# Performance work log

Hardware: AMD Instinct MI355X
Metric: run time of the kernel (lower is better)

## Reference

```python
import jax, jax.numpy as jnp
import numpy as np

H_IMG, W_IMG = 32, 32   # image_size -> seq_len = 1024
NH, HD, D = 8, 32, 256  # num_heads, head_dim, d_model
B = 8


def _relative_positions(h, w):
    # Swin-style relative position index table, [h*w, h*w] int32
    y = np.arange(h); x = np.arange(w)
    coords = np.stack(np.meshgrid(y, x, indexing='ij')).reshape(2, -1)  # [2, S]
    rel = coords[:, :, None] - coords[:, None, :]                      # [2, S, S]
    rel = rel.transpose(1, 2, 0).astype(np.int64)                      # [S, S, 2]
    rel[:, :, 0] += h - 1
    rel[:, :, 1] += w - 1
    rel[:, :, 0] *= 2 * w - 1
    return np.int32(rel.sum(-1))                                       # [S, S]

_POS = _relative_positions(H_IMG, W_IMG)


def setup_inputs() -> dict:
    key = jax.random.key(0)
    ks = jax.random.split(key, 8)
    S = H_IMG * W_IMG
    return {
        'inputs_q': jax.random.normal(ks[0], (B, S, D), jnp.float32),
        'inputs_kv': jax.random.normal(ks[1], (B, S, D), jnp.float32),
        'Wq': jax.random.normal(ks[2], (D, NH, HD), jnp.float32) / np.sqrt(D),
        'bq': jnp.zeros((NH, HD), jnp.float32),
        'Wk': jax.random.normal(ks[3], (D, NH, HD), jnp.float32) / np.sqrt(D),
        'bk': jnp.zeros((NH, HD), jnp.float32),
        'Wv': jax.random.normal(ks[4], (D, NH, HD), jnp.float32) / np.sqrt(D),
        'bv': jnp.zeros((NH, HD), jnp.float32),
        'rel_table': 0.02 * jax.random.normal(ks[5], ((2 * H_IMG - 1) * (2 * W_IMG - 1), NH), jnp.float32),
        'Wo': jax.random.normal(ks[6], (NH, HD, D), jnp.float32) / np.sqrt(NH * HD),
        'bo': jnp.zeros((D,), jnp.float32),
    }


def reference(inputs_q, inputs_kv, Wq, bq, Wk, bk, Wv, bv, rel_table, Wo, bo):
    pos = jnp.asarray(_POS)                                  # [S, S] int32 (constant)
    q = jnp.einsum('bsd,dhk->bshk', inputs_q, Wq) + bq       # [B, S, H, HD]
    k = jnp.einsum('bsd,dhk->bshk', inputs_kv, Wk) + bk
    v = jnp.einsum('bsd,dhk->bshk', inputs_kv, Wv) + bv
    q = q / jnp.sqrt(jnp.asarray(HD, q.dtype))
    attn = jnp.einsum('bqhd,bkhd->bhqk', q, k)               # [B, H, S, S]
    rel_bias = rel_table[pos]                                # [S, S, H]
    attn = attn + jnp.transpose(rel_bias, (2, 0, 1))[None]   # broadcast over batch
    attn = jax.nn.softmax(attn, axis=-1)
    x = jnp.einsum('bhqk,bkhd->bqhd', attn, v)               # [B, S, H, HD]
    return jnp.einsum('bqhd,hdf->bqf', x, Wo) + bo           # [B, S, D]
```

## Files before the change

kernel.cpp:

```cpp
#include <hip/hip_runtime.h>

#define B_SZ   8
#define S_LEN  1024
#define D_MOD  256
#define NHEADS 8
#define M_ROWS 8192
#define LOG2E  1.4426950408889634f
#define QSCALE_LOG2E 0.2550352766751165f

typedef _Float16 f16x8 __attribute__((ext_vector_type(8)));
typedef _Float16 f16x4 __attribute__((ext_vector_type(4)));
typedef float    f32x4 __attribute__((ext_vector_type(4)));

__global__ __launch_bounds__(256)
void prep_kernel(const float* __restrict__ Wq, const float* __restrict__ Wk,
                 const float* __restrict__ Wv, const float* __restrict__ Wo,
                 const float* __restrict__ rel,
                 _Float16* __restrict__ wtp, float* __restrict__ tab) {
    if (blockIdx.x < 32) {
        __shared__ _Float16 Wl[32 * 264];
        const int mi = blockIdx.x >> 3;
        const int k0 = (blockIdx.x & 7) << 5;
        const float* W = (mi == 0) ? Wq : (mi == 1) ? Wk : (mi == 2) ? Wv : Wo;
        {
            const int r  = threadIdx.x >> 3;
            const int c4 = (threadIdx.x & 7) * 4;
            const float* src = W + (size_t)(k0 + r) * 256 + c4;
#pragma unroll
            for (int g = 0; g < 8; ++g) {
                f32x4 v = *(const f32x4*)(src + g * 32);
                f16x4 o;
#pragma unroll
                for (int j = 0; j < 4; ++j) o[j] = (_Float16)v[j];
                *(f16x4*)(&Wl[r * 264 + c4 + g * 32]) = o;
            }
        }
        __syncthreads();
        const int n16 = threadIdx.x >> 4;
        const int l16 = threadIdx.x & 15;
        const int kk  = k0 >> 5;
#pragma unroll
        for (int quad = 0; quad < 4; ++quad) {
            f16x8 v;
#pragma unroll
            for (int j = 0; j < 8; ++j) v[j] = Wl[(quad * 8 + j) * 264 + n16 * 16 + l16];
            *(f16x8*)(wtp + (((size_t)(mi * 16 + n16) * 8 + kk) << 9) + (quad * 16 + l16) * 8) = v;
        }
        return;
    }
    __shared__ float rl[63 * 8];
    const int dy31 = blockIdx.x - 32;
    for (int f = threadIdx.x; f < 504; f += 256) rl[f] = rel[(size_t)dy31 * 504 + f];
    __syncthreads();
    const int h  = threadIdx.x >> 5;
    const int r5 = threadIdx.x & 31;
#pragma unroll
    for (int c = 0; c < 6; ++c) {
        const int oi   = r5 * 6 + c;
        const int e    = oi >> 6;
        const int lane = oi & 63;
        const int quad = lane >> 4, l16 = lane & 15;
        f32x4 v;
#pragma unroll
        for (int reg = 0; reg < 4; ++reg) {
            const int idx = 16 * e + l16 - quad * 4 - reg + 15;
            v[reg] = rl[idx * 8 + h] * LOG2E;
        }
        *(f32x4*)(tab + (((size_t)(h * 63 + dy31) * 3 + e) << 8) + lane * 4) = v;
    }
}

__global__ __launch_bounds__(256)
void gemm_qkv_kernel(const float* __restrict__ in_q, const float* __restrict__ in_kv,
                     const _Float16* __restrict__ wtp,
                     const float* __restrict__ bq, const float* __restrict__ bk,
                     const float* __restrict__ bv,
                     _Float16* __restrict__ qs, _Float16* __restrict__ ks,
                     _Float16* __restrict__ vs) {
    __shared__ __align__(16) _Float16 As[64 * 264];
    _Float16* Ta = As;
    _Float16* Tb = As + 64 * 72;

    const int tid  = threadIdx.x;
    const int w    = tid >> 6;
    const int lane = tid & 63;
    const int quad = lane >> 4;
    const int l16  = lane & 15;
    const int m0 = blockIdx.x * 64, n0 = blockIdx.y * 64, z = blockIdx.z;
    const int b = m0 >> 10, mloc = m0 & 1023;

    {
        const int r  = tid >> 2;
        const int c4 = (tid & 3) * 4;
        const float* src = (z ? in_kv : in_q) + (size_t)(m0 + r) * 256 + c4;
        _Float16* dst = As + r * 264 + c4;
#pragma unroll
        for (int g = 0; g < 16; ++g) {
            f32x4 v = *(const f32x4*)(src + g * 16);
            f16x4 o;
#pragma unroll
            for (int j = 0; j < 4; ++j) o[j] = (_Float16)v[j];
            *(f16x4*)(dst + g * 16) = o;
        }
    }
    __syncthreads();

    const int n16base = (n0 >> 4) + (w >> 1) * 2;
    const int mA = z ? 1 : 0;
    const _Float16* wA0 = wtp + (((size_t)(mA * 16 + n16base + 0) * 8) << 9) + lane * 8;
    const _Float16* wA1 = wtp + (((size_t)(mA * 16 + n16base + 1) * 8) << 9) + lane * 8;
    const _Float16* wV0 = wtp + (((size_t)(2 * 16 + n16base + 0) * 8) << 9) + lane * 8;
    const _Float16* wV1 = wtp + (((size_t)(2 * 16 + n16base + 1) * 8) << 9) + lane * 8;
    const _Float16* arow0 = As + ((w & 1) * 32 + l16) * 264;
    const _Float16* arow1 = arow0 + 16 * 264;

    f32x4 accA[2][2], accV[2][2];
#pragma unroll
    for (int i = 0; i < 2; ++i)
#pragma unroll
        for (int j = 0; j < 2; ++j) {
            accA[i][j] = (f32x4){0.f, 0.f, 0.f, 0.f};
            accV[i][j] = (f32x4){0.f, 0.f, 0.f, 0.f};
        }

#pragma unroll
    for (int kk = 0; kk < 8; ++kk) {
        const int k8 = kk * 32 + quad * 8;
        f16x8 a0 = *(const f16x8*)(arow0 + k8);
        f16x8 a1 = *(const f16x8*)(arow1 + k8);
        f16x8 w0 = *(const f16x8*)(wA0 + kk * 512);
        f16x8 w1 = *(const f16x8*)(wA1 + kk * 512);
        accA[0][0] = __builtin_amdgcn_mfma_f32_16x16x32_f16(w0, a0, accA[0][0], 0, 0, 0);
        accA[0][1] = __builtin_amdgcn_mfma_f32_16x16x32_f16(w0, a1, accA[0][1], 0, 0, 0);
        accA[1][0] = __builtin_amdgcn_mfma_f32_16x16x32_f16(w1, a0, accA[1][0], 0, 0, 0);
        accA[1][1] = __builtin_amdgcn_mfma_f32_16x16x32_f16(w1, a1, accA[1][1], 0, 0, 0);
        if (z == 1) {
            f16x8 v0 = *(const f16x8*)(wV0 + kk * 512);
            f16x8 v1 = *(const f16x8*)(wV1 + kk * 512);
            accV[0][0] = __builtin_amdgcn_mfma_f32_16x16x32_f16(a0, v0, accV[0][0], 0, 0, 0);
            accV[0][1] = __builtin_amdgcn_mfma_f32_16x16x32_f16(a0, v1, accV[0][1], 0, 0, 0);
            accV[1][0] = __builtin_amdgcn_mfma_f32_16x16x32_f16(a1, v0, accV[1][0], 0, 0, 0);
            accV[1][1] = __builtin_amdgcn_mfma_f32_16x16x32_f16(a1, v1, accV[1][1], 0, 0, 0);
        }
    }
    __syncthreads();

    {
        const float* biasA = z ? bk : bq;
        const float  sc    = z ? 1.0f : QSCALE_LOG2E;
#pragma unroll
        for (int i = 0; i < 2; ++i) {
            f32x4 b4 = *(const f32x4*)(biasA + n0 + (w >> 1) * 32 + i * 16 + quad * 4);
#pragma unroll
            for (int jj = 0; jj < 2; ++jj) {
                f16x4 pk;
#pragma unroll
                for (int r = 0; r < 4; ++r) pk[r] = (_Float16)((accA[i][jj][r] + b4[r]) * sc);
                *(f16x4*)(Ta + ((w & 1) * 32 + jj * 16 + l16) * 72 +
                               (w >> 1) * 32 + i * 16 + quad * 4) = pk;
            }
        }
        if (z == 1) {
#pragma unroll
            for (int i = 0; i < 2; ++i) {
                const float bvv = bv[n0 + (w >> 1) * 32 + i * 16 + l16];
#pragma unroll
                for (int jj = 0; jj < 2; ++jj) {
                    f16x4 pk;
#pragma unroll
                    for (int r = 0; r < 4; ++r) pk[r] = (_Float16)(accV[jj][i][r] + bvv);
                    *(f16x4*)(Tb + ((w >> 1) * 32 + i * 16 + l16) * 72 +
                                   (w & 1) * 32 + jj * 16 + quad * 4) = pk;
                }
            }
        }
    }
    __syncthreads();
    {
        const int l16c = tid & 15, qdc = (tid >> 4) & 3;
        const int tile0 = mloc >> 5;
#pragma unroll
        for (int c2i = 0; c2i < 2; ++c2i) {
            const int c2 = w * 2 + c2i;
            const int s2 = c2 >> 2, sub = (c2 >> 1) & 1, hs = c2 & 1;
            const int bh = b * 8 + (n0 >> 5) + hs;
            const size_t dbase = (((size_t)(bh * 32 + tile0 + s2) * 2 + sub) << 9) + lane * 8;
            f16x8 va = *(const f16x8*)(Ta + (s2 * 32 + sub * 16 + l16c) * 72 +
                                            hs * 32 + qdc * 8);
            *(f16x8*)((z ? ks : qs) + dbase) = va;
            if (z == 1) {
                f16x8 vb = *(const f16x8*)(Tb + (hs * 32 + sub * 16 + l16c) * 72 +
                                                s2 * 32 + qdc * 8);
                *(f16x8*)(vs + dbase) = vb;
            }
        }
    }
}

__global__ __launch_bounds__(256)
void gemm_out_kernel(const _Float16* __restrict__ xh, const _Float16* __restrict__ wtp,
                     const float* __restrict__ bo, float* __restrict__ out) {
    __shared__ __align__(16) _Float16 As[64 * 264];
    const int tid  = threadIdx.x;
    const int w    = tid >> 6;
    const int lane = tid & 63;
    const int quad = lane >> 4;
    const int l16  = lane & 15;
    const int m0 = blockIdx.x * 64, n0 = blockIdx.y * 64;

    {
        const int r  = tid >> 2;
        const int c8 = (tid & 3) * 8;
        const _Float16* src = xh + (size_t)(m0 + r) * 256 + c8;
        _Float16* dst = As + r * 264 + c8;
#pragma unroll
        for (int g = 0; g < 8; ++g)
            *(f16x8*)(dst + g * 32) = *(const f16x8*)(src + g * 32);
    }
    __syncthreads();

    const int n16base = 48 + (n0 >> 4) + (w >> 1) * 2;
    const _Float16* w0p = wtp + (((size_t)(n16base + 0) * 8) << 9) + lane * 8;
    const _Float16* w1p = wtp + (((size_t)(n16base + 1) * 8) << 9) + lane * 8;
    const _Float16* arow0 = As + ((w & 1) * 32 + l16) * 264;
    const _Float16* arow1 = arow0 + 16 * 264;

    f32x4 acc[2][2];
#pragma unroll
    for (int i = 0; i < 2; ++i)
#pragma unroll
        for (int j = 0; j < 2; ++j) acc[i][j] = (f32x4){0.f, 0.f, 0.f, 0.f};

#pragma unroll
    for (int kk = 0; kk < 8; ++kk) {
        const int k8 = kk * 32 + quad * 8;
        f16x8 a0 = *(const f16x8*)(arow0 + k8);
        f16x8 a1 = *(const f16x8*)(arow1 + k8);
        f16x8 b0 = *(const f16x8*)(w0p + kk * 512);
        f16x8 b1 = *(const f16x8*)(w1p + kk * 512);
        acc[0][0] = __builtin_amdgcn_mfma_f32_16x16x32_f16(a0, b0, acc[0][0], 0, 0, 0);
        acc[0][1] = __builtin_amdgcn_mfma_f32_16x16x32_f16(a0, b1, acc[0][1], 0, 0, 0);
        acc[1][0] = __builtin_amdgcn_mfma_f32_16x16x32_f16(a1, b0, acc[1][0], 0, 0, 0);
        acc[1][1] = __builtin_amdgcn_mfma_f32_16x16x32_f16(a1, b1, acc[1][1], 0, 0, 0);
    }

#pragma unroll
    for (int i = 0; i < 2; ++i) {
        const int col = n0 + (w >> 1) * 32 + i * 16 + l16;
        const float bvv = bo[col];
#pragma unroll
        for (int jj = 0; jj < 2; ++jj) {
#pragma unroll
            for (int r = 0; r < 4; ++r) {
                const int row = m0 + (w & 1) * 32 + jj * 16 + quad * 4 + r;
                out[(size_t)row * 256 + col] = acc[jj][i][r] + bvv;
            }
        }
    }
}

__global__ __launch_bounds__(256)
void attn_kernel(const _Float16* __restrict__ qs, const _Float16* __restrict__ ks,
                 const _Float16* __restrict__ vs, const float* __restrict__ tab,
                 _Float16* __restrict__ xh) {
    __shared__ __align__(16) _Float16 Ps[4][32][40];

    const int tid  = threadIdx.x;
    const int w    = tid >> 6;
    const int lane = tid & 63;
    const int quad = lane >> 4;
    const int l16  = lane & 15;

    const int n     = blockIdx.x;
    const int xcd   = n & 7;
    const int local = n >> 3;
    const int bh    = xcd * 8 + (local & 7);
    const int qc    = local >> 3;
    const int b = bh >> 3, h = bh & 7;
    const int qrow_base = qc * 128 + w * 32;
    const int yq = qc * 4 + w;

    const _Float16* qp = qs + (((size_t)(bh * 32 + yq) * 2) << 9) + lane * 8;
    const f16x8 qf0 = *(const f16x8*)(qp);
    const f16x8 qf1 = *(const f16x8*)(qp + 512);
    const _Float16* kp = ks + (((size_t)bh * 64) << 9) + lane * 8;
    const _Float16* vp = vs + (((size_t)bh * 64) << 9) + lane * 8;
    const float* tb = tab + (((size_t)h * 63 * 3) << 8) + lane * 4;

    f16x8 ones;
#pragma unroll
    for (int j = 0; j < 8; ++j) ones[j] = (_Float16)1.0f;

    f32x4 o00 = {0.f,0.f,0.f,0.f}, o01 = {0.f,0.f,0.f,0.f};
    f32x4 o10 = {0.f,0.f,0.f,0.f}, o11 = {0.f,0.f,0.f,0.f};
    f32x4 ol0 = {0.f,0.f,0.f,0.f}, ol1 = {0.f,0.f,0.f,0.f};

    f16x8 kf0 = *(const f16x8*)(kp);
    f16x8 kf1 = *(const f16x8*)(kp + 512);
    f16x8 vf0 = *(const f16x8*)(vp);
    f16x8 vf1 = *(const f16x8*)(vp + 512);
    f32x4 c0 = *(const f32x4*)(tb + (yq + 31) * 768);
    f32x4 c1 = *(const f32x4*)(tb + (yq + 31) * 768 + 256);
    f32x4 c2 = *(const f32x4*)(tb + (yq + 31) * 768 + 512);

    for (int kt = 0; kt < 32; ++kt) {
        const bool more = (kt < 31);
        f16x8 nk0, nk1, nv0, nv1;
        f32x4 nc0, nc1, nc2;
        if (more) {
            const _Float16* kq = kp + (kt + 1) * 1024;
            nk0 = *(const f16x8*)(kq);
            nk1 = *(const f16x8*)(kq + 512);
            const _Float16* vq = vp + (kt + 1) * 1024;
            nv0 = *(const f16x8*)(vq);
            nv1 = *(const f16x8*)(vq + 512);
            const int d = (yq + 30 - kt) * 768;
            nc0 = *(const f32x4*)(tb + d);
            nc1 = *(const f32x4*)(tb + d + 256);
            nc2 = *(const f32x4*)(tb + d + 512);
        }

        f32x4 s00 = __builtin_amdgcn_mfma_f32_16x16x32_f16(kf0, qf0, c1, 0, 0, 0);
        f32x4 s01 = __builtin_amdgcn_mfma_f32_16x16x32_f16(kf1, qf0, c0, 0, 0, 0);
        f32x4 s10 = __builtin_amdgcn_mfma_f32_16x16x32_f16(kf0, qf1, c2, 0, 0, 0);
        f32x4 s11 = __builtin_amdgcn_mfma_f32_16x16x32_f16(kf1, qf1, c1, 0, 0, 0);

        f16x4 p;
#pragma unroll
        for (int r = 0; r < 4; ++r) p[r] = (_Float16)__builtin_amdgcn_exp2f(s00[r]);
        *(f16x4*)(&Ps[w][l16][quad * 4]) = p;
#pragma unroll
        for (int r = 0; r < 4; ++r) p[r] = (_Float16)__builtin_amdgcn_exp2f(s01[r]);
        *(f16x4*)(&Ps[w][l16][16 + quad * 4]) = p;
#pragma unroll
        for (int r = 0; r < 4; ++r) p[r] = (_Float16)__builtin_amdgcn_exp2f(s10[r]);
        *(f16x4*)(&Ps[w][16 + l16][quad * 4]) = p;
#pragma unroll
        for (int r = 0; r < 4; ++r) p[r] = (_Float16)__builtin_amdgcn_exp2f(s11[r]);
        *(f16x4*)(&Ps[w][16 + l16][16 + quad * 4]) = p;

        const f16x8 pf0 = *(const f16x8*)(&Ps[w][l16][quad * 8]);
        const f16x8 pf1 = *(const f16x8*)(&Ps[w][16 + l16][quad * 8]);
        o00 = __builtin_amdgcn_mfma_f32_16x16x32_f16(vf0, pf0, o00, 0, 0, 0);
        o01 = __builtin_amdgcn_mfma_f32_16x16x32_f16(vf0, pf1, o01, 0, 0, 0);
        o10 = __builtin_amdgcn_mfma_f32_16x16x32_f16(vf1, pf0, o10, 0, 0, 0);
        o11 = __builtin_amdgcn_mfma_f32_16x16x32_f16(vf1, pf1, o11, 0, 0, 0);
        ol0 = __builtin_amdgcn_mfma_f32_16x16x32_f16(ones, pf0, ol0, 0, 0, 0);
        ol1 = __builtin_amdgcn_mfma_f32_16x16x32_f16(ones, pf1, ol1, 0, 0, 0);

        if (more) {
            kf0 = nk0; kf1 = nk1; vf0 = nv0; vf1 = nv1;
            c0 = nc0; c1 = nc1; c2 = nc2;
        }
    }

#pragma unroll
    for (int qh = 0; qh < 2; ++qh) {
        const f32x4 onl = qh ? o01 : o00;
        const f32x4 onh = qh ? o11 : o10;
        const f32x4 ll  = qh ? ol1 : ol0;
        const float inv = __builtin_amdgcn_rcpf(ll[0]);
        const int qg = qrow_base + qh * 16 + l16;
        f16x4 u, v;
#pragma unroll
        for (int r = 0; r < 4; ++r) {
            u[r] = (_Float16)(onl[r] * inv);
            v[r] = (_Float16)(onh[r] * inv);
        }
        _Float16* op = xh + ((size_t)(b * S_LEN + qg)) * D_MOD + h * 32 + quad * 4;
        *(f16x4*)(op)      = u;
        *(f16x4*)(op + 16) = v;
    }
}

extern "C" void kernel_launch(void* const* d_in, const int* in_sizes, int n_in,
                              void* d_out, int out_size, void* d_ws, size_t ws_size,
                              hipStream_t stream) {
    const float* in_q  = (const float*)d_in[0];
    const float* in_kv = (const float*)d_in[1];
    const float* Wq    = (const float*)d_in[2];
    const float* bq    = (const float*)d_in[3];
    const float* Wk    = (const float*)d_in[4];
    const float* bk    = (const float*)d_in[5];
    const float* Wv    = (const float*)d_in[6];
    const float* bv    = (const float*)d_in[7];
    const float* rel   = (const float*)d_in[8];
    const float* Wo    = (const float*)d_in[9];
    const float* bo    = (const float*)d_in[10];
    float* out = (float*)d_out;

    char* wsb = (char*)d_ws;
    _Float16* qs  = (_Float16*)(wsb);
    _Float16* ks  = (_Float16*)(wsb + (size_t)4  * 1048576);
    _Float16* vs  = (_Float16*)(wsb + (size_t)8  * 1048576);
    _Float16* xh  = (_Float16*)(wsb + (size_t)12 * 1048576);
    _Float16* wtp = (_Float16*)(wsb + (size_t)16 * 1048576);
    float*    tab = (float*)   (wsb + (size_t)17 * 1048576);

    const dim3 blk(256);

    prep_kernel<<<dim3(95), blk, 0, stream>>>(Wq, Wk, Wv, Wo, rel, wtp, tab);
    gemm_qkv_kernel<<<dim3(128, 4, 2), blk, 0, stream>>>(
        in_q, in_kv, wtp, bq, bk, bv, qs, ks, vs);
    attn_kernel<<<dim3(512), blk, 0, stream>>>(qs, ks, vs, tab, xh);
    gemm_out_kernel<<<dim3(128, 4), blk, 0, stream>>>(xh, wtp, bo, out);
}
```

Baseline: 124.1 us.

## Store bias table in fp16, retile QKV GEMM, write attention output in MFMA layout

The relative-position bias table is now stored in fp16 and converted to float inside the attention loop, which halves the bytes it reads per tile. The QKV projection is retiled so each block handles 32 rows across the full 256 output columns for one of Q, K or V, on a grid of 256 by 3. The attention kernel now writes its output already packed in MFMA fragment order, so the output GEMM can read fragments straight from global memory and no longer stages them in LDS. The costs are some extra conversion instructions in the attention loop and fp16 rounding of the bias values.

Measured after the change: 127.3 us. 2.6% more time.

```diff
diff --git a/kernel.cpp b/kernel.cpp
--- a/kernel.cpp
+++ b/kernel.cpp
@@ -4,7 +4,6 @@
 #define S_LEN  1024
 #define D_MOD  256
 #define NHEADS 8
-#define M_ROWS 8192
 #define LOG2E  1.4426950408889634f
 #define QSCALE_LOG2E 0.2550352766751165f
 
@@ -16,7 +15,7 @@
 void prep_kernel(const float* __restrict__ Wq, const float* __restrict__ Wk,
                  const float* __restrict__ Wv, const float* __restrict__ Wo,
                  const float* __restrict__ rel,
-                 _Float16* __restrict__ wtp, float* __restrict__ tab) {
+                 _Float16* __restrict__ wtp, _Float16* __restrict__ tabh) {
     if (blockIdx.x < 32) {
         __shared__ _Float16 Wl[32 * 264];
         const int mi = blockIdx.x >> 3;
@@ -60,13 +59,13 @@
         const int e    = oi >> 6;
         const int lane = oi & 63;
         const int quad = lane >> 4, l16 = lane & 15;
-        f32x4 v;
+        f16x4 v;
 #pragma unroll
         for (int reg = 0; reg < 4; ++reg) {
             const int idx = 16 * e + l16 - quad * 4 - reg + 15;
-            v[reg] = rl[idx * 8 + h] * LOG2E;
-        }
-        *(f32x4*)(tab + (((size_t)(h * 63 + dy31) * 3 + e) << 8) + lane * 4) = v;
+            v[reg] = (_Float16)(rl[idx * 8 + h] * LOG2E);
+        }
+        *(f16x4*)(tabh + (((size_t)(h * 63 + dy31) * 3 + e) << 8) + lane * 4) = v;
     }
 }
 
@@ -77,153 +76,115 @@
                      const float* __restrict__ bv,
                      _Float16* __restrict__ qs, _Float16* __restrict__ ks,
                      _Float16* __restrict__ vs) {
-    __shared__ __align__(16) _Float16 As[64 * 264];
-    _Float16* Ta = As;
-    _Float16* Tb = As + 64 * 72;
-
+    __shared__ __align__(16) _Float16 Lds[256 * 40];
     const int tid  = threadIdx.x;
     const int w    = tid >> 6;
     const int lane = tid & 63;
     const int quad = lane >> 4;
     const int l16  = lane & 15;
-    const int m0 = blockIdx.x * 64, n0 = blockIdx.y * 64, z = blockIdx.z;
-    const int b = m0 >> 10, mloc = m0 & 1023;
+    const int mt = blockIdx.x;
+    const int z  = blockIdx.y;
+    const int m0 = mt * 32;
+    const int b  = mt >> 5, t = mt & 31;
 
     {
-        const int r  = tid >> 2;
-        const int c4 = (tid & 3) * 4;
+        const int r  = tid >> 3;
+        const int c4 = (tid & 7) * 4;
         const float* src = (z ? in_kv : in_q) + (size_t)(m0 + r) * 256 + c4;
-        _Float16* dst = As + r * 264 + c4;
-#pragma unroll
-        for (int g = 0; g < 16; ++g) {
-            f32x4 v = *(const f32x4*)(src + g * 16);
+        _Float16* dst = Lds + r * 264 + c4;
+#pragma unroll
+        for (int g = 0; g < 8; ++g) {
+            f32x4 v = *(const f32x4*)(src + g * 32);
             f16x4 o;
 #pragma unroll
             for (int j = 0; j < 4; ++j) o[j] = (_Float16)v[j];
-            *(f16x4*)(dst + g * 16) = o;
+            *(f16x4*)(dst + g * 32) = o;
         }
     }
     __syncthreads();
 
-    const int n16base = (n0 >> 4) + (w >> 1) * 2;
-    const int mA = z ? 1 : 0;
-    const _Float16* wA0 = wtp + (((size_t)(mA * 16 + n16base + 0) * 8) << 9) + lane * 8;
-    const _Float16* wA1 = wtp + (((size_t)(mA * 16 + n16base + 1) * 8) << 9) + lane * 8;
-    const _Float16* wV0 = wtp + (((size_t)(2 * 16 + n16base + 0) * 8) << 9) + lane * 8;
-    const _Float16* wV1 = wtp + (((size_t)(2 * 16 + n16base + 1) * 8) << 9) + lane * 8;
-    const _Float16* arow0 = As + ((w & 1) * 32 + l16) * 264;
-    const _Float16* arow1 = arow0 + 16 * 264;
-
-    f32x4 accA[2][2], accV[2][2];
-#pragma unroll
-    for (int i = 0; i < 2; ++i)
-#pragma unroll
-        for (int j = 0; j < 2; ++j) {
-            accA[i][j] = (f32x4){0.f, 0.f, 0.f, 0.f};
-            accV[i][j] = (f32x4){0.f, 0.f, 0.f, 0.f};
-        }
+    f32x4 acc[2][4];
+#pragma unroll
+    for (int jj = 0; jj < 2; ++jj)
+#pragma unroll
+        for (int i = 0; i < 4; ++i) acc[jj][i] = (f32x4){0.f, 0.f, 0.f, 0.f};
 
 #pragma unroll
     for (int kk = 0; kk < 8; ++kk) {
         const int k8 = kk * 32 + quad * 8;
-        f16x8 a0 = *(const f16x8*)(arow0 + k8);
-        f16x8 a1 = *(const f16x8*)(arow1 + k8);
-        f16x8 w0 = *(const f16x8*)(wA0 + kk * 512);
-        f16x8 w1 = *(const f16x8*)(wA1 + kk * 512);
-        accA[0][0] = __builtin_amdgcn_mfma_f32_16x16x32_f16(w0, a0, accA[0][0], 0, 0, 0);
-        accA[0][1] = __builtin_amdgcn_mfma_f32_16x16x32_f16(w0, a1, accA[0][1], 0, 0, 0);
-        accA[1][0] = __builtin_amdgcn_mfma_f32_16x16x32_f16(w1, a0, accA[1][0], 0, 0, 0);
-        accA[1][1] = __builtin_amdgcn_mfma_f32_16x16x32_f16(w1, a1, accA[1][1], 0, 0, 0);
-        if (z == 1) {
-            f16x8 v0 = *(const f16x8*)(wV0 + kk * 512);
-            f16x8 v1 = *(const f16x8*)(wV1 + kk * 512);
-            accV[0][0] = __builtin_amdgcn_mfma_f32_16x16x32_f16(a0, v0, accV[0][0], 0, 0, 0);
-            accV[0][1] = __builtin_amdgcn_mfma_f32_16x16x32_f16(a0, v1, accV[0][1], 0, 0, 0);
-            accV[1][0] = __builtin_amdgcn_mfma_f32_16x16x32_f16(a1, v0, accV[1][0], 0, 0, 0);
-            accV[1][1] = __builtin_amdgcn_mfma_f32_16x16x32_f16(a1, v1, accV[1][1], 0, 0, 0);
+        f16x8 a0 = *(const f16x8*)(Lds + l16 * 264 + k8);
+        f16x8 a1 = *(const f16x8*)(Lds + (16 + l16) * 264 + k8);
+#pragma unroll
+        for (int i = 0; i < 4; ++i) {
+            f16x8 wv = *(const f16x8*)(wtp + (((size_t)(z * 16 + w * 4 + i) * 8 + kk) << 9) + lane * 8);
+            if (z < 2) {
+                acc[0][i] = __builtin_amdgcn_mfma_f32_16x16x32_f16(wv, a0, acc[0][i], 0, 0, 0);
+                acc[1][i] = __builtin_amdgcn_mfma_f32_16x16x32_f16(wv, a1, acc[1][i], 0, 0, 0);
+            } else {
+                acc[0][i] = __builtin_amdgcn_mfma_f32_16x16x32_f16(a0, wv, acc[0][i], 0, 0, 0);
+                acc[1][i] = __builtin_amdgcn_mfma_f32_16x16x32_f16(a1, wv, acc[1][i], 0, 0, 0);
+            }
         }
     }
     __syncthreads();
 
-    {
-        const float* biasA = z ? bk : bq;
-        const float  sc    = z ? 1.0f : QSCALE_LOG2E;
-#pragma unroll
-        for (int i = 0; i < 2; ++i) {
-            f32x4 b4 = *(const f32x4*)(biasA + n0 + (w >> 1) * 32 + i * 16 + quad * 4);
+    if (z < 2) {
+        const float* bias = z ? bk : bq;
+        const float  sc   = z ? 1.0f : QSCALE_LOG2E;
+#pragma unroll
+        for (int i = 0; i < 4; ++i) {
+            f32x4 b4 = *(const f32x4*)(bias + (w * 4 + i) * 16 + quad * 4);
 #pragma unroll
             for (int jj = 0; jj < 2; ++jj) {
                 f16x4 pk;
 #pragma unroll
-                for (int r = 0; r < 4; ++r) pk[r] = (_Float16)((accA[i][jj][r] + b4[r]) * sc);
-                *(f16x4*)(Ta + ((w & 1) * 32 + jj * 16 + l16) * 72 +
-                               (w >> 1) * 32 + i * 16 + quad * 4) = pk;
-            }
-        }
-        if (z == 1) {
-#pragma unroll
-            for (int i = 0; i < 2; ++i) {
-                const float bvv = bv[n0 + (w >> 1) * 32 + i * 16 + l16];
-#pragma unroll
-                for (int jj = 0; jj < 2; ++jj) {
-                    f16x4 pk;
-#pragma unroll
-                    for (int r = 0; r < 4; ++r) pk[r] = (_Float16)(accV[jj][i][r] + bvv);
-                    *(f16x4*)(Tb + ((w >> 1) * 32 + i * 16 + l16) * 72 +
-                                   (w & 1) * 32 + jj * 16 + quad * 4) = pk;
-                }
-            }
-        }
-    }
-    __syncthreads();
-    {
-        const int l16c = tid & 15, qdc = (tid >> 4) & 3;
-        const int tile0 = mloc >> 5;
-#pragma unroll
-        for (int c2i = 0; c2i < 2; ++c2i) {
-            const int c2 = w * 2 + c2i;
-            const int s2 = c2 >> 2, sub = (c2 >> 1) & 1, hs = c2 & 1;
-            const int bh = b * 8 + (n0 >> 5) + hs;
-            const size_t dbase = (((size_t)(bh * 32 + tile0 + s2) * 2 + sub) << 9) + lane * 8;
-            f16x8 va = *(const f16x8*)(Ta + (s2 * 32 + sub * 16 + l16c) * 72 +
-                                            hs * 32 + qdc * 8);
-            *(f16x8*)((z ? ks : qs) + dbase) = va;
-            if (z == 1) {
-                f16x8 vb = *(const f16x8*)(Tb + (hs * 32 + sub * 16 + l16c) * 72 +
-                                                s2 * 32 + qdc * 8);
-                *(f16x8*)(vs + dbase) = vb;
-            }
+                for (int r = 0; r < 4; ++r) pk[r] = (_Float16)((acc[jj][i][r] + b4[r]) * sc);
+                *(f16x4*)(Lds + (jj * 16 + l16) * 264 + (w * 4 + i) * 16 + quad * 4) = pk;
+            }
+        }
+        __syncthreads();
+        _Float16* dst = z ? ks : qs;
+#pragma unroll
+        for (int c = 0; c < 4; ++c) {
+            const int sg = w * 4 + c;
+            const int sub = sg >> 3, h = sg & 7;
+            f16x8 v = *(const f16x8*)(Lds + (sub * 16 + l16) * 264 + h * 32 + quad * 8);
+            *(f16x8*)(dst + (((size_t)((b * 8 + h) * 32 + t) * 2 + sub) << 9) + lane * 8) = v;
+        }
+    } else {
+#pragma unroll
+        for (int i = 0; i < 4; ++i) {
+            const float bvv = bv[(w * 4 + i) * 16 + l16];
+#pragma unroll
+            for (int jj = 0; jj < 2; ++jj) {
+                f16x4 pk;
+#pragma unroll
+                for (int r = 0; r < 4; ++r) pk[r] = (_Float16)(acc[jj][i][r] + bvv);
+                *(f16x4*)(Lds + ((w * 4 + i) * 16 + l16) * 40 + jj * 16 + quad * 4) = pk;
+            }
+        }
+        __syncthreads();
+#pragma unroll
+        for (int c = 0; c < 4; ++c) {
+            const int sg = w * 4 + c;
+            const int sub = sg >> 3, h = sg & 7;
+            f16x8 v = *(const f16x8*)(Lds + (h * 32 + sub * 16 + l16) * 40 + quad * 8);
+            *(f16x8*)(vs + (((size_t)((b * 8 + h) * 32 + t) * 2 + sub) << 9) + lane * 8) = v;
         }
     }
 }
 
 __global__ __launch_bounds__(256)
-void gemm_out_kernel(const _Float16* __restrict__ xh, const _Float16* __restrict__ wtp,
+void gemm_out_kernel(const _Float16* __restrict__ xs, const _Float16* __restrict__ wtp,
                      const float* __restrict__ bo, float* __restrict__ out) {
-    __shared__ __align__(16) _Float16 As[64 * 264];
     const int tid  = threadIdx.x;
     const int w    = tid >> 6;
     const int lane = tid & 63;
     const int quad = lane >> 4;
     const int l16  = lane & 15;
-    const int m0 = blockIdx.x * 64, n0 = blockIdx.y * 64;
-
-    {
-        const int r  = tid >> 2;
-        const int c8 = (tid & 3) * 8;
-        const _Float16* src = xh + (size_t)(m0 + r) * 256 + c8;
-        _Float16* dst = As + r * 264 + c8;
-#pragma unroll
-        for (int g = 0; g < 8; ++g)
-            *(f16x8*)(dst + g * 32) = *(const f16x8*)(src + g * 32);
-    }
-    __syncthreads();
-
-    const int n16base = 48 + (n0 >> 4) + (w >> 1) * 2;
-    const _Float16* w0p = wtp + (((size_t)(n16base + 0) * 8) << 9) + lane * 8;
-    const _Float16* w1p = wtp + (((size_t)(n16base + 1) * 8) << 9) + lane * 8;
-    const _Float16* arow0 = As + ((w & 1) * 32 + l16) * 264;
-    const _Float16* arow1 = arow0 + 16 * 264;
+    const int bx = blockIdx.x, by = blockIdx.y;
+    const int mt0  = bx * 4 + (w & 1) * 2;
+    const int n16a = by * 4 + (w >> 1) * 2;
 
     f32x4 acc[2][2];
 #pragma unroll
@@ -233,11 +194,10 @@
 
 #pragma unroll
     for (int kk = 0; kk < 8; ++kk) {
-        const int k8 = kk * 32 + quad * 8;
-        f16x8 a0 = *(const f16x8*)(arow0 + k8);
-        f16x8 a1 = *(const f16x8*)(arow1 + k8);
-        f16x8 b0 = *(const f16x8*)(w0p + kk * 512);
-        f16x8 b1 = *(const f16x8*)(w1p + kk * 512);
+        f16x8 a0 = *(const f16x8*)(xs + (((size_t)(mt0 + 0) * 8 + kk) << 9) + lane * 8);
+        f16x8 a1 = *(const f16x8*)(xs + (((size_t)(mt0 + 1) * 8 + kk) << 9) + lane * 8);
+        f16x8 b0 = *(const f16x8*)(wtp + (((size_t)(48 + n16a + 0) * 8 + kk) << 9) + lane * 8);
+        f16x8 b1 = *(const f16x8*)(wtp + (((size_t)(48 + n16a + 1) * 8 + kk) << 9) + lane * 8);
         acc[0][0] = __builtin_amdgcn_mfma_f32_16x16x32_f16(a0, b0, acc[0][0], 0, 0, 0);
         acc[0][1] = __builtin_amdgcn_mfma_f32_16x16x32_f16(a0, b1, acc[0][1], 0, 0, 0);
         acc[1][0] = __builtin_amdgcn_mfma_f32_16x16x32_f16(a1, b0, acc[1][0], 0, 0, 0);
@@ -246,13 +206,13 @@
 
 #pragma unroll
     for (int i = 0; i < 2; ++i) {
-        const int col = n0 + (w >> 1) * 32 + i * 16 + l16;
+        const int col = (n16a + i) * 16 + l16;
         const float bvv = bo[col];
 #pragma unroll
         for (int jj = 0; jj < 2; ++jj) {
 #pragma unroll
             for (int r = 0; r < 4; ++r) {
-                const int row = m0 + (w & 1) * 32 + jj * 16 + quad * 4 + r;
+                const int row = (mt0 + jj) * 16 + quad * 4 + r;
                 out[(size_t)row * 256 + col] = acc[jj][i][r] + bvv;
             }
         }
@@ -261,8 +221,8 @@
 
 __global__ __launch_bounds__(256)
 void attn_kernel(const _Float16* __restrict__ qs, const _Float16* __restrict__ ks,
-                 const _Float16* __restrict__ vs, const float* __restrict__ tab,
-                 _Float16* __restrict__ xh) {
+                 const _Float16* __restrict__ vs, const _Float16* __restrict__ tabh,
+                 _Float16* __restrict__ xs) {
     __shared__ __align__(16) _Float16 Ps[4][32][40];
 
     const int tid  = threadIdx.x;
@@ -285,7 +245,7 @@
     const f16x8 qf1 = *(const f16x8*)(qp + 512);
     const _Float16* kp = ks + (((size_t)bh * 64) << 9) + lane * 8;
     const _Float16* vp = vs + (((size_t)bh * 64) << 9) + lane * 8;
-    const float* tb = tab + (((size_t)h * 63 * 3) << 8) + lane * 4;
+    const _Float16* tb = tabh + (((size_t)h * 189) << 8) + lane * 4;
 
     f16x8 ones;
 #pragma unroll
@@ -299,14 +259,21 @@
     f16x8 kf1 = *(const f16x8*)(kp + 512);
     f16x8 vf0 = *(const f16x8*)(vp);
     f16x8 vf1 = *(const f16x8*)(vp + 512);
-    f32x4 c0 = *(const f32x4*)(tb + (yq + 31) * 768);
-    f32x4 c1 = *(const f32x4*)(tb + (yq + 31) * 768 + 256);
-    f32x4 c2 = *(const f32x4*)(tb + (yq + 31) * 768 + 512);
+    f32x4 c0, c1, c2;
+    {
+        f16x4 t0 = *(const f16x4*)(tb + (((yq + 31) * 3 + 0) << 8));
+        f16x4 t1 = *(const f16x4*)(tb + (((yq + 31) * 3 + 1) << 8));
+        f16x4 t2 = *(const f16x4*)(tb + (((yq + 31) * 3 + 2) << 8));
+#pragma unroll
+        for (int r = 0; r < 4; ++r) {
+            c0[r] = (float)t0[r]; c1[r] = (float)t1[r]; c2[r] = (float)t2[r];
+        }
+    }
 
     for (int kt = 0; kt < 32; ++kt) {
         const bool more = (kt < 31);
         f16x8 nk0, nk1, nv0, nv1;
-        f32x4 nc0, nc1, nc2;
+        f16x4 nt0, nt1, nt2;
         if (more) {
             const _Float16* kq = kp + (kt + 1) * 1024;
             nk0 = *(const f16x8*)(kq);
@@ -314,10 +281,10 @@
             const _Float16* vq = vp + (kt + 1) * 1024;
             nv0 = *(const f16x8*)(vq);
             nv1 = *(const f16x8*)(vq + 512);
-            const int d = (yq + 30 - kt) * 768;
-            nc0 = *(const f32x4*)(tb + d);
-            nc1 = *(const f32x4*)(tb + d + 256);
-            nc2 = *(const f32x4*)(tb + d + 512);
+            const int d = (yq + 30 - kt) * 3;
+            nt0 = *(const f16x4*)(tb + ((d + 0) << 8));
+            nt1 = *(const f16x4*)(tb + ((d + 1) << 8));
+            nt2 = *(const f16x4*)(tb + ((d + 2) << 8));
         }
 
         f32x4 s00 = __builtin_amdgcn_mfma_f32_16x16x32_f16(kf0, qf0, c1, 0, 0, 0);
@@ -350,26 +317,33 @@
 
         if (more) {
             kf0 = nk0; kf1 = nk1; vf0 = nv0; vf1 = nv1;
-            c0 = nc0; c1 = nc1; c2 = nc2;
-        }
-    }
-
-#pragma unroll
-    for (int qh = 0; qh < 2; ++qh) {
-        const f32x4 onl = qh ? o01 : o00;
-        const f32x4 onh = qh ? o11 : o10;
-        const f32x4 ll  = qh ? ol1 : ol0;
+#pragma unroll
+            for (int r = 0; r < 4; ++r) {
+                c0[r] = (float)nt0[r]; c1[r] = (float)nt1[r]; c2[r] = (float)nt2[r];
+            }
+        }
+    }
+
+#pragma unroll
+    for (int qsub = 0; qsub < 2; ++qsub) {
+        const f32x4 olo = qsub ? o01 : o00;
+        const f32x4 ohi = qsub ? o11 : o10;
+        const f32x4 ll  = qsub ? ol1 : ol0;
         const float inv = __builtin_amdgcn_rcpf(ll[0]);
-        const int qg = qrow_base + qh * 16 + l16;
         f16x4 u, v;
 #pragma unroll
         for (int r = 0; r < 4; ++r) {
-            u[r] = (_Float16)(onl[r] * inv);
-            v[r] = (_Float16)(onh[r] * inv);
-        }
-        _Float16* op = xh + ((size_t)(b * S_LEN + qg)) * D_MOD + h * 32 + quad * 4;
-        *(f16x4*)(op)      = u;
-        *(f16x4*)(op + 16) = v;
+            u[r] = (_Float16)(olo[r] * inv);
+            v[r] = (_Float16)(ohi[r] * inv);
+        }
+        *(f16x4*)(&Ps[w][qsub * 16 + l16][quad * 4]) = u;
+        *(f16x4*)(&Ps[w][qsub * 16 + l16][16 + quad * 4]) = v;
+    }
+#pragma unroll
+    for (int qsub = 0; qsub < 2; ++qsub) {
+        f16x8 af = *(const f16x8*)(&Ps[w][qsub * 16 + l16][quad * 8]);
+        const int mtile = b * 64 + qc * 8 + w * 2 + qsub;
+        *(f16x8*)(xs + (((size_t)mtile * 8 + h) << 9) + lane * 8) = af;
     }
 }
 
@@ -390,18 +364,18 @@
     float* out = (float*)d_out;
 
     char* wsb = (char*)d_ws;
-    _Float16* qs  = (_Float16*)(wsb);
-    _Float16* ks  = (_Float16*)(wsb + (size_t)4  * 1048576);
-    _Float16* vs  = (_Float16*)(wsb + (size_t)8  * 1048576);
-    _Float16* xh  = (_Float16*)(wsb + (size_t)12 * 1048576);
-    _Float16* wtp = (_Float16*)(wsb + (size_t)16 * 1048576);
-    float*    tab = (float*)   (wsb + (size_t)17 * 1048576);
+    _Float16* qs   = (_Float16*)(wsb);
+    _Float16* ks   = (_Float16*)(wsb + (size_t)4  * 1048576);
+    _Float16* vs   = (_Float16*)(wsb + (size_t)8  * 1048576);
+    _Float16* xs   = (_Float16*)(wsb + (size_t)12 * 1048576);
+    _Float16* wtp  = (_Float16*)(wsb + (size_t)16 * 1048576);
+    _Float16* tabh = (_Float16*)(wsb + (size_t)17 * 1048576);
 
     const dim3 blk(256);
 
-    prep_kernel<<<dim3(95), blk, 0, stream>>>(Wq, Wk, Wv, Wo, rel, wtp, tab);
-    gemm_qkv_kernel<<<dim3(128, 4, 2), blk, 0, stream>>>(
+    prep_kernel<<<dim3(95), blk, 0, stream>>>(Wq, Wk, Wv, Wo, rel, wtp, tabh);
+    gemm_qkv_kernel<<<dim3(256, 3), blk, 0, stream>>>(
         in_q, in_kv, wtp, bq, bk, bv, qs, ks, vs);
-    attn_kernel<<<dim3(512), blk, 0, stream>>>(qs, ks, vs, tab, xh);
-    gemm_out_kernel<<<dim3(128, 4), blk, 0, stream>>>(xh, wtp, bo, out);
-}
+    attn_kernel<<<dim3(512), blk, 0, stream>>>(qs, ks, vs, tabh, xs);
+    gemm_out_kernel<<<dim3(128, 4), blk, 0, stream>>>(xs, wtp, bo, out);
+}
```
